# Kernel optimization log

Hardware: AMD Instinct MI355X
Metric: run time of the kernel (lower is better)

The kernel has to match this reference:

```python
import jax, jax.numpy as jnp
import numpy as np

B, C, H, W = 4, 256, 128, 256
CQK = C // 4   # 64
COUT = 256


def setup_inputs() -> dict:
    key = jax.random.key(0)
    ks = jax.random.split(key, 8)
    s = 0.05
    return {
        "flow": jax.random.normal(ks[0], (B, C, H, W), jnp.float32),
        "de_out": jax.random.normal(ks[1], (B, C, H, W), jnp.float32),
        "Wq": jax.random.normal(ks[2], (CQK, C), jnp.float32) * s,
        "bq": jax.random.normal(ks[3], (CQK,), jnp.float32) * s,
        "Wk": jax.random.normal(ks[4], (CQK, C), jnp.float32) * s,
        "bk": jax.random.normal(ks[5], (CQK,), jnp.float32) * s,
        "Wv": jax.random.normal(ks[6], (COUT, C), jnp.float32) * s,
        "bv": jax.random.normal(ks[7], (COUT,), jnp.float32) * s,
    }


def reference(flow, de_out, Wq, bq, Wk, bk, Wv, bv):
    # 1x1 convs == channel-mixing einsums
    q = jnp.einsum('bchw,dc->bdhw', de_out, Wq) + bq[None, :, None, None]  # [B,CQK,H,W]
    k = jnp.einsum('bchw,dc->bdhw', flow, Wk) + bk[None, :, None, None]   # [B,CQK,H,W]
    v = jnp.einsum('bchw,oc->bohw', flow, Wv) + bv[None, :, None, None]   # [B,COUT,H,W]
    # width-axial attention: energy[b,h,w,w'] = sum_d q[b,d,h,w]*k[b,d,h,w']
    energy = jnp.einsum('bdhw,bdhv->bhwv', q, k)          # [B,H,W,W]
    att = jax.nn.softmax(energy, axis=-1)                 # softmax over key width w'
    # out[b,o,h,w] = sum_{w'} v[b,o,h,w'] * att[b,h,w,w']
    out = jnp.einsum('bohv,bhwv->bohw', v, att)           # [B,COUT,H,W]
    return out
```

## Files before the change

kernel.cpp:

```cpp
#include <hip/hip_runtime.h>

#define Bn   4
#define Cc   256
#define Hh   128
#define Ww   256
#define HWp  32768
#define CQK  64
#define COUT 256

typedef _Float16 half8 __attribute__((ext_vector_type(8)));
typedef _Float16 half4 __attribute__((ext_vector_type(4)));
typedef float   floatx4 __attribute__((ext_vector_type(4)));

#define MFMA16(a, b, c) __builtin_amdgcn_mfma_f32_16x16x32_f16((a), (b), (c), 0, 0, 0)

__global__ __launch_bounds__(256) void k_qkv(
    const float* __restrict__ flow, const float* __restrict__ de_out,
    const float* __restrict__ Wq, const float* __restrict__ bq,
    const float* __restrict__ Wk, const float* __restrict__ bk,
    const float* __restrict__ Wv, const float* __restrict__ bv,
    _Float16* __restrict__ Qws, _Float16* __restrict__ Kws,
    _Float16* __restrict__ Vws)
{
    __shared__ __align__(16) _Float16 x_lds[64 * 264];
    __shared__ __align__(16) _Float16 w_lds[32 * 264];

    const int t   = threadIdx.x;
    const int b   = blockIdx.y;
    const int job = blockIdx.z;
    const int pb  = blockIdx.x * 64;

    const float* X = (job == 0 ? de_out : flow) + (size_t)b * Cc * HWp;

    {
        const int px4 = t & 15;
        const int cg  = t >> 4;
        for (int rep = 0; rep < 4; ++rep) {
            const int c0 = 4 * cg + 64 * rep;
            float4 r0 = *(const float4*)&X[(size_t)(c0 + 0) * HWp + pb + 4 * px4];
            float4 r1 = *(const float4*)&X[(size_t)(c0 + 1) * HWp + pb + 4 * px4];
            float4 r2 = *(const float4*)&X[(size_t)(c0 + 2) * HWp + pb + 4 * px4];
            float4 r3 = *(const float4*)&X[(size_t)(c0 + 3) * HWp + pb + 4 * px4];
            half4 h;
            h = (half4){(_Float16)r0.x, (_Float16)r1.x, (_Float16)r2.x, (_Float16)r3.x};
            *(half4*)&x_lds[(4 * px4 + 0) * 264 + c0] = h;
            h = (half4){(_Float16)r0.y, (_Float16)r1.y, (_Float16)r2.y, (_Float16)r3.y};
            *(half4*)&x_lds[(4 * px4 + 1) * 264 + c0] = h;
            h = (half4){(_Float16)r0.z, (_Float16)r1.z, (_Float16)r2.z, (_Float16)r3.z};
            *(half4*)&x_lds[(4 * px4 + 2) * 264 + c0] = h;
            h = (half4){(_Float16)r0.w, (_Float16)r1.w, (_Float16)r2.w, (_Float16)r3.w};
            *(half4*)&x_lds[(4 * px4 + 3) * 264 + c0] = h;
        }
    }

    const int nmt  = (job == 0) ? 2 : 10;
    const int wv   = t >> 6;
    const int lane = t & 63;
    const int quad = lane >> 4;
    const int l16  = lane & 15;

    for (int mt = 0; mt < nmt; ++mt) {
        const float* Wsel;
        const float* bsel;
        int mbase, dstmode;
        _Float16* dst;
        if (job == 0)      { Wsel = Wq; bsel = bq; mbase = mt * 32;        dst = Qws; dstmode = 0; }
        else if (mt < 2)   { Wsel = Wk; bsel = bk; mbase = mt * 32;        dst = Kws; dstmode = 0; }
        else               { Wsel = Wv; bsel = bv; mbase = (mt - 2) * 32;  dst = Vws; dstmode = 1; }

        __syncthreads();
        for (int i = 0; i < 8; ++i) {
            const int f4  = t + 256 * i;
            const int row = f4 >> 6;
            const int off = (f4 & 63) * 4;
            float4 w4 = *(const float4*)&Wsel[(size_t)(mbase + row) * 256 + off];
            half4 h = (half4){(_Float16)w4.x, (_Float16)w4.y, (_Float16)w4.z, (_Float16)w4.w};
            *(half4*)&w_lds[row * 264 + off] = h;
        }
        __syncthreads();

        const int mrow = 16 * (wv & 1) + l16;
        half8 a[8];
        for (int ks = 0; ks < 8; ++ks)
            a[ks] = *(const half8*)&w_lds[mrow * 264 + ks * 32 + quad * 8];

        const int n0 = (wv >> 1) * 32;
        floatx4 acc0 = {0.f, 0.f, 0.f, 0.f};
        floatx4 acc1 = {0.f, 0.f, 0.f, 0.f};
        for (int ks = 0; ks < 8; ++ks) {
            half8 b0 = *(const half8*)&x_lds[(n0 + l16) * 264 + ks * 32 + quad * 8];
            half8 b1 = *(const half8*)&x_lds[(n0 + 16 + l16) * 264 + ks * 32 + quad * 8];
            acc0 = MFMA16(a[ks], b0, acc0);
            acc1 = MFMA16(a[ks], b1, acc1);
        }

        const int mloc = 16 * (wv & 1) + quad * 4;
        float4 bi = *(const float4*)&bsel[mbase + mloc];
        const float bia[4] = {bi.x, bi.y, bi.z, bi.w};
        if (dstmode == 0) {
            for (int nt = 0; nt < 2; ++nt) {
                floatx4 acc = nt ? acc1 : acc0;
                const int pix = pb + n0 + nt * 16 + l16;
                half4 h = (half4){(_Float16)(acc[0] + bia[0]), (_Float16)(acc[1] + bia[1]),
                                  (_Float16)(acc[2] + bia[2]), (_Float16)(acc[3] + bia[3])};
                *(half4*)&dst[((size_t)b * HWp + pix) * 64 + mt * 32 + mloc] = h;
            }
        } else {
            for (int nt = 0; nt < 2; ++nt) {
                floatx4 acc = nt ? acc1 : acc0;
                const int pix = pb + n0 + nt * 16 + l16;
                for (int r = 0; r < 4; ++r) {
                    const int o = mbase + mloc + r;
                    dst[((size_t)b * 256 + o) * HWp + pix] = (_Float16)(acc[r] + bia[r]);
                }
            }
        }
    }
}

__global__ __launch_bounds__(256) void k_attn(
    const _Float16* __restrict__ Qws, const _Float16* __restrict__ Kws,
    const _Float16* __restrict__ Vws, float* __restrict__ out)
{
    __shared__ __align__(16) _Float16 q_lds[32 * 72];
    __shared__ __align__(16) _Float16 k_lds[256 * 72];
    __shared__ __align__(16) _Float16 att_lds[32 * 264];
    __shared__ float inv_l[32];

    const int t    = threadIdx.x;
    const int h    = blockIdx.x;
    const int b    = blockIdx.y;
    const int wv   = t >> 6;
    const int lane = t & 63;
    const int quad = lane >> 4;
    const int l16  = lane & 15;
    const size_t pixbase = (size_t)b * HWp + h * 256;

    for (int chunk = 0; chunk < 8; ++chunk) {
        __syncthreads();
        {
            const int row = t >> 3, off = (t & 7) * 8;
            *(half8*)&q_lds[row * 72 + off] =
                *(const half8*)&Qws[(pixbase + chunk * 32 + row) * 64 + off];
        }
        for (int i = 0; i < 8; ++i) {
            const int g = t + 256 * i;
            const int row = g >> 3, off = (g & 7) * 8;
            *(half8*)&k_lds[row * 72 + off] =
                *(const half8*)&Kws[(pixbase + row) * 64 + off];
        }
        __syncthreads();

        {
            const int mrow = 16 * (wv & 1) + l16;
            half8 a0 = *(const half8*)&q_lds[mrow * 72 + quad * 8];
            half8 a1 = *(const half8*)&q_lds[mrow * 72 + 32 + quad * 8];
            const int mb2 = 16 * (wv & 1) + quad * 4;
            for (int j = 0; j < 8; ++j) {
                const int nt = (wv >> 1) * 8 + j;
                half8 b0 = *(const half8*)&k_lds[(nt * 16 + l16) * 72 + quad * 8];
                half8 b1 = *(const half8*)&k_lds[(nt * 16 + l16) * 72 + 32 + quad * 8];
                floatx4 acc = {0.f, 0.f, 0.f, 0.f};
                acc = MFMA16(a0, b0, acc);
                acc = MFMA16(a1, b1, acc);
                for (int r = 0; r < 4; ++r)
                    att_lds[(mb2 + r) * 264 + nt * 16 + l16] = (_Float16)acc[r];
            }
        }
        __syncthreads();

        {
            const int r = t >> 3, seg = t & 7;
            _Float16* rowp = &att_lds[r * 264 + seg * 32];
            float vals[32];
            float mx = -1e30f;
            for (int i = 0; i < 32; ++i) { vals[i] = (float)rowp[i]; mx = fmaxf(mx, vals[i]); }
            mx = fmaxf(mx, __shfl_xor(mx, 1));
            mx = fmaxf(mx, __shfl_xor(mx, 2));
            mx = fmaxf(mx, __shfl_xor(mx, 4));
            float s = 0.f;
            for (int i = 0; i < 32; ++i) { vals[i] = __expf(vals[i] - mx); s += vals[i]; }
            s += __shfl_xor(s, 1);
            s += __shfl_xor(s, 2);
            s += __shfl_xor(s, 4);
            for (int i = 0; i < 32; ++i) rowp[i] = (_Float16)vals[i];
            if (seg == 0) inv_l[r] = 1.f / s;
        }
        __syncthreads();

        _Float16* v_lds = k_lds;
        for (int os = 0; os < 4; ++os) {
            if (os) __syncthreads();
            for (int i = 0; i < 8; ++i) {
                const int g = t + 256 * i;
                const int row = g >> 5, off = (g & 31) * 8;
                *(half8*)&v_lds[row * 264 + off] =
                    *(const half8*)&Vws[((size_t)b * 256 + os * 64 + row) * HWp + h * 256 + off];
            }
            __syncthreads();

            floatx4 acc0 = {0.f, 0.f, 0.f, 0.f};
            floatx4 acc1 = {0.f, 0.f, 0.f, 0.f};
            for (int ks = 0; ks < 8; ++ks) {
                half8 a  = *(const half8*)&v_lds[(16 * wv + l16) * 264 + ks * 32 + quad * 8];
                half8 b0 = *(const half8*)&att_lds[l16 * 264 + ks * 32 + quad * 8];
                half8 b1 = *(const half8*)&att_lds[(16 + l16) * 264 + ks * 32 + quad * 8];
                acc0 = MFMA16(a, b0, acc0);
                acc1 = MFMA16(a, b1, acc1);
            }
            const float il0 = inv_l[l16];
            const float il1 = inv_l[16 + l16];
            const int og = os * 64 + 16 * wv + quad * 4;
            const int wg = chunk * 32 + l16;
            for (int r = 0; r < 4; ++r) {
                out[(((size_t)b * 256 + og + r) * Hh + h) * Ww + wg]      = acc0[r] * il0;
                out[(((size_t)b * 256 + og + r) * Hh + h) * Ww + 16 + wg] = acc1[r] * il1;
            }
        }
    }
}

extern "C" void kernel_launch(void* const* d_in, const int* in_sizes, int n_in,
                              void* d_out, int out_size, void* d_ws, size_t ws_size,
                              hipStream_t stream)
{
    const float* flow   = (const float*)d_in[0];
    const float* de_out = (const float*)d_in[1];
    const float* Wq = (const float*)d_in[2];
    const float* bq = (const float*)d_in[3];
    const float* Wk = (const float*)d_in[4];
    const float* bk = (const float*)d_in[5];
    const float* Wv = (const float*)d_in[6];
    const float* bv = (const float*)d_in[7];

    _Float16* Qws = (_Float16*)d_ws;
    _Float16* Kws = Qws + (size_t)Bn * HWp * 64;
    _Float16* Vws = Kws + (size_t)Bn * HWp * 64;
    float* out = (float*)d_out;

    dim3 g1(HWp / 64, Bn, 2);
    k_qkv<<<g1, 256, 0, stream>>>(flow, de_out, Wq, bq, Wk, bk, Wv, bv, Qws, Kws, Vws);

    dim3 g2(Hh, Bn);
    k_attn<<<g2, 256, 0, stream>>>(Qws, Kws, Vws, out);
}
```

Before: 452.8 us.

## Use 32x32 MFMA and 64-row query chunks in attention, drop weight LDS staging in QKV

```diff
diff --git a/kernel.cpp b/kernel.cpp
--- a/kernel.cpp
+++ b/kernel.cpp
@@ -10,11 +10,13 @@
 
 typedef _Float16 half8 __attribute__((ext_vector_type(8)));
 typedef _Float16 half4 __attribute__((ext_vector_type(4)));
-typedef float   floatx4 __attribute__((ext_vector_type(4)));
+typedef float   floatx4  __attribute__((ext_vector_type(4)));
+typedef float   floatx16 __attribute__((ext_vector_type(16)));
 
 #define MFMA16(a, b, c) __builtin_amdgcn_mfma_f32_16x16x32_f16((a), (b), (c), 0, 0, 0)
-
-__global__ __launch_bounds__(256) void k_qkv(
+#define MFMA32(a, b, c) __builtin_amdgcn_mfma_f32_32x32x16_f16((a), (b), (c), 0, 0, 0)
+
+__global__ __launch_bounds__(256, 4) void k_qkv(
     const float* __restrict__ flow, const float* __restrict__ de_out,
     const float* __restrict__ Wq, const float* __restrict__ bq,
     const float* __restrict__ Wk, const float* __restrict__ bk,
@@ -23,7 +25,6 @@
     _Float16* __restrict__ Vws)
 {
     __shared__ __align__(16) _Float16 x_lds[64 * 264];
-    __shared__ __align__(16) _Float16 w_lds[32 * 264];
 
     const int t   = threadIdx.x;
     const int b   = blockIdx.y;
@@ -34,83 +35,65 @@
 
     {
         const int px4 = t & 15;
-        const int cg  = t >> 4;
-        for (int rep = 0; rep < 4; ++rep) {
-            const int c0 = 4 * cg + 64 * rep;
-            float4 r0 = *(const float4*)&X[(size_t)(c0 + 0) * HWp + pb + 4 * px4];
-            float4 r1 = *(const float4*)&X[(size_t)(c0 + 1) * HWp + pb + 4 * px4];
-            float4 r2 = *(const float4*)&X[(size_t)(c0 + 2) * HWp + pb + 4 * px4];
-            float4 r3 = *(const float4*)&X[(size_t)(c0 + 3) * HWp + pb + 4 * px4];
-            half4 h;
-            h = (half4){(_Float16)r0.x, (_Float16)r1.x, (_Float16)r2.x, (_Float16)r3.x};
-            *(half4*)&x_lds[(4 * px4 + 0) * 264 + c0] = h;
-            h = (half4){(_Float16)r0.y, (_Float16)r1.y, (_Float16)r2.y, (_Float16)r3.y};
-            *(half4*)&x_lds[(4 * px4 + 1) * 264 + c0] = h;
-            h = (half4){(_Float16)r0.z, (_Float16)r1.z, (_Float16)r2.z, (_Float16)r3.z};
-            *(half4*)&x_lds[(4 * px4 + 2) * 264 + c0] = h;
-            h = (half4){(_Float16)r0.w, (_Float16)r1.w, (_Float16)r2.w, (_Float16)r3.w};
-            *(half4*)&x_lds[(4 * px4 + 3) * 264 + c0] = h;
+        const int c8  = t >> 4;
+        for (int rep = 0; rep < 2; ++rep) {
+            const int c0 = 8 * c8 + 128 * rep;
+            float4 r[8];
+            #pragma unroll
+            for (int j = 0; j < 8; ++j)
+                r[j] = *(const float4*)&X[(size_t)(c0 + j) * HWp + pb + 4 * px4];
+            #pragma unroll
+            for (int i = 0; i < 4; ++i) {
+                half8 h;
+                #pragma unroll
+                for (int j = 0; j < 8; ++j) h[j] = (_Float16)((&r[j].x)[i]);
+                *(half8*)&x_lds[(4 * px4 + i) * 264 + c0] = h;
+            }
         }
     }
-
-    const int nmt  = (job == 0) ? 2 : 10;
+    __syncthreads();
+
     const int wv   = t >> 6;
     const int lane = t & 63;
     const int quad = lane >> 4;
     const int l16  = lane & 15;
-
-    for (int mt = 0; mt < nmt; ++mt) {
-        const float* Wsel;
-        const float* bsel;
-        int mbase, dstmode;
-        _Float16* dst;
-        if (job == 0)      { Wsel = Wq; bsel = bq; mbase = mt * 32;        dst = Qws; dstmode = 0; }
-        else if (mt < 2)   { Wsel = Wk; bsel = bk; mbase = mt * 32;        dst = Kws; dstmode = 0; }
-        else               { Wsel = Wv; bsel = bv; mbase = (mt - 2) * 32;  dst = Vws; dstmode = 1; }
-
-        __syncthreads();
-        for (int i = 0; i < 8; ++i) {
-            const int f4  = t + 256 * i;
-            const int row = f4 >> 6;
-            const int off = (f4 & 63) * 4;
-            float4 w4 = *(const float4*)&Wsel[(size_t)(mbase + row) * 256 + off];
-            half4 h = (half4){(_Float16)w4.x, (_Float16)w4.y, (_Float16)w4.z, (_Float16)w4.w};
-            *(half4*)&w_lds[row * 264 + off] = h;
-        }
-        __syncthreads();
-
-        const int mrow = 16 * (wv & 1) + l16;
+    const int ntiles = (job == 0) ? 1 : 5;
+
+    for (int tt = 0; tt < ntiles; ++tt) {
+        const float* Wsel; const float* bsel; _Float16* dst; int m0, mode;
+        if (job == 0)    { Wsel = Wq; bsel = bq; dst = Qws; m0 = 16 * wv;              mode = 0; }
+        else if (tt==0)  { Wsel = Wk; bsel = bk; dst = Kws; m0 = 16 * wv;              mode = 0; }
+        else             { Wsel = Wv; bsel = bv; dst = Vws; m0 = 64 * (tt-1) + 16*wv;  mode = 1; }
+
         half8 a[8];
-        for (int ks = 0; ks < 8; ++ks)
-            a[ks] = *(const half8*)&w_lds[mrow * 264 + ks * 32 + quad * 8];
-
-        const int n0 = (wv >> 1) * 32;
-        floatx4 acc0 = {0.f, 0.f, 0.f, 0.f};
-        floatx4 acc1 = {0.f, 0.f, 0.f, 0.f};
+        const float* wrow = &Wsel[(size_t)(m0 + l16) * 256];
+        #pragma unroll
         for (int ks = 0; ks < 8; ++ks) {
-            half8 b0 = *(const half8*)&x_lds[(n0 + l16) * 264 + ks * 32 + quad * 8];
-            half8 b1 = *(const half8*)&x_lds[(n0 + 16 + l16) * 264 + ks * 32 + quad * 8];
-            acc0 = MFMA16(a[ks], b0, acc0);
-            acc1 = MFMA16(a[ks], b1, acc1);
-        }
-
-        const int mloc = 16 * (wv & 1) + quad * 4;
-        float4 bi = *(const float4*)&bsel[mbase + mloc];
+            float4 wa = *(const float4*)&wrow[ks * 32 + quad * 8];
+            float4 wb = *(const float4*)&wrow[ks * 32 + quad * 8 + 4];
+            a[ks] = (half8){(_Float16)wa.x, (_Float16)wa.y, (_Float16)wa.z, (_Float16)wa.w,
+                            (_Float16)wb.x, (_Float16)wb.y, (_Float16)wb.z, (_Float16)wb.w};
+        }
+        float4 bi = *(const float4*)&bsel[m0 + quad * 4];
         const float bia[4] = {bi.x, bi.y, bi.z, bi.w};
-        if (dstmode == 0) {
-            for (int nt = 0; nt < 2; ++nt) {
-                floatx4 acc = nt ? acc1 : acc0;
-                const int pix = pb + n0 + nt * 16 + l16;
+
+        #pragma unroll
+        for (int nt = 0; nt < 4; ++nt) {
+            floatx4 acc = {0.f, 0.f, 0.f, 0.f};
+            #pragma unroll
+            for (int ks = 0; ks < 8; ++ks) {
+                half8 bf = *(const half8*)&x_lds[(nt * 16 + l16) * 264 + ks * 32 + quad * 8];
+                acc = MFMA16(a[ks], bf, acc);
+            }
+            const int pix = pb + nt * 16 + l16;
+            if (mode == 0) {
                 half4 h = (half4){(_Float16)(acc[0] + bia[0]), (_Float16)(acc[1] + bia[1]),
                                   (_Float16)(acc[2] + bia[2]), (_Float16)(acc[3] + bia[3])};
-                *(half4*)&dst[((size_t)b * HWp + pix) * 64 + mt * 32 + mloc] = h;
-            }
-        } else {
-            for (int nt = 0; nt < 2; ++nt) {
-                floatx4 acc = nt ? acc1 : acc0;
-                const int pix = pb + n0 + nt * 16 + l16;
+                *(half4*)&dst[((size_t)b * HWp + pix) * 64 + m0 + quad * 4] = h;
+            } else {
+                #pragma unroll
                 for (int r = 0; r < 4; ++r) {
-                    const int o = mbase + mloc + r;
+                    const int o = m0 + quad * 4 + r;
                     dst[((size_t)b * 256 + o) * HWp + pix] = (_Float16)(acc[r] + bia[r]);
                 }
             }
@@ -118,103 +101,124 @@
     }
 }
 
-__global__ __launch_bounds__(256) void k_attn(
+__global__ __launch_bounds__(256, 2) void k_attn(
     const _Float16* __restrict__ Qws, const _Float16* __restrict__ Kws,
     const _Float16* __restrict__ Vws, float* __restrict__ out)
 {
-    __shared__ __align__(16) _Float16 q_lds[32 * 72];
-    __shared__ __align__(16) _Float16 k_lds[256 * 72];
-    __shared__ __align__(16) _Float16 att_lds[32 * 264];
-    __shared__ float inv_l[32];
+    __shared__ __align__(16) _Float16 kv_lds[256 * 72];
+    __shared__ __align__(16) _Float16 att_lds[64 * 264];
+    __shared__ float inv_l[64];
 
     const int t    = threadIdx.x;
     const int h    = blockIdx.x;
     const int b    = blockIdx.y;
     const int wv   = t >> 6;
     const int lane = t & 63;
-    const int quad = lane >> 4;
-    const int l16  = lane & 15;
+    const int hi   = lane >> 5;
+    const int l32  = lane & 31;
     const size_t pixbase = (size_t)b * HWp + h * 256;
 
-    for (int chunk = 0; chunk < 8; ++chunk) {
-        __syncthreads();
-        {
-            const int row = t >> 3, off = (t & 7) * 8;
-            *(half8*)&q_lds[row * 72 + off] =
-                *(const half8*)&Qws[(pixbase + chunk * 32 + row) * 64 + off];
-        }
+    for (int chunk = 0; chunk < 4; ++chunk) {
+        __syncthreads();
+        #pragma unroll
         for (int i = 0; i < 8; ++i) {
             const int g = t + 256 * i;
             const int row = g >> 3, off = (g & 7) * 8;
-            *(half8*)&k_lds[row * 72 + off] =
+            *(half8*)&kv_lds[row * 72 + off] =
                 *(const half8*)&Kws[(pixbase + row) * 64 + off];
         }
         __syncthreads();
 
         {
-            const int mrow = 16 * (wv & 1) + l16;
-            half8 a0 = *(const half8*)&q_lds[mrow * 72 + quad * 8];
-            half8 a1 = *(const half8*)&q_lds[mrow * 72 + 32 + quad * 8];
-            const int mb2 = 16 * (wv & 1) + quad * 4;
-            for (int j = 0; j < 8; ++j) {
-                const int nt = (wv >> 1) * 8 + j;
-                half8 b0 = *(const half8*)&k_lds[(nt * 16 + l16) * 72 + quad * 8];
-                half8 b1 = *(const half8*)&k_lds[(nt * 16 + l16) * 72 + 32 + quad * 8];
-                floatx4 acc = {0.f, 0.f, 0.f, 0.f};
-                acc = MFMA16(a0, b0, acc);
-                acc = MFMA16(a1, b1, acc);
-                for (int r = 0; r < 4; ++r)
-                    att_lds[(mb2 + r) * 264 + nt * 16 + l16] = (_Float16)acc[r];
-            }
-        }
-        __syncthreads();
-
-        {
-            const int r = t >> 3, seg = t & 7;
-            _Float16* rowp = &att_lds[r * 264 + seg * 32];
+            const int mt = wv & 1;
+            half8 aq[4];
+            #pragma unroll
+            for (int ks = 0; ks < 4; ++ks)
+                aq[ks] = *(const half8*)&Qws[(pixbase + chunk*64 + mt*32 + l32) * 64
+                                             + ks * 16 + hi * 8];
+            #pragma unroll
+            for (int j = 0; j < 4; ++j) {
+                const int n0 = (4 * (wv >> 1) + j) * 32;
+                floatx16 acc = {};
+                #pragma unroll
+                for (int ks = 0; ks < 4; ++ks) {
+                    half8 bk8 = *(const half8*)&kv_lds[(n0 + l32) * 72 + ks * 16 + hi * 8];
+                    acc = MFMA32(aq[ks], bk8, acc);
+                }
+                #pragma unroll
+                for (int r = 0; r < 16; ++r) {
+                    const int row = mt * 32 + (r & 3) + 8 * (r >> 2) + 4 * hi;
+                    att_lds[row * 264 + n0 + l32] = (_Float16)acc[r];
+                }
+            }
+        }
+        __syncthreads();
+
+        #pragma unroll
+        for (int p = 0; p < 2; ++p) {
+            const int row = 32 * p + (t >> 3), seg = t & 7;
+            _Float16* rowp = &att_lds[row * 264 + seg * 32];
             float vals[32];
             float mx = -1e30f;
-            for (int i = 0; i < 32; ++i) { vals[i] = (float)rowp[i]; mx = fmaxf(mx, vals[i]); }
+            #pragma unroll
+            for (int i8 = 0; i8 < 4; ++i8) {
+                half8 hv = *(const half8*)&rowp[i8 * 8];
+                #pragma unroll
+                for (int j = 0; j < 8; ++j) {
+                    vals[i8 * 8 + j] = (float)hv[j];
+                    mx = fmaxf(mx, vals[i8 * 8 + j]);
+                }
+            }
             mx = fmaxf(mx, __shfl_xor(mx, 1));
             mx = fmaxf(mx, __shfl_xor(mx, 2));
             mx = fmaxf(mx, __shfl_xor(mx, 4));
             float s = 0.f;
+            #pragma unroll
             for (int i = 0; i < 32; ++i) { vals[i] = __expf(vals[i] - mx); s += vals[i]; }
             s += __shfl_xor(s, 1);
             s += __shfl_xor(s, 2);
             s += __shfl_xor(s, 4);
-            for (int i = 0; i < 32; ++i) rowp[i] = (_Float16)vals[i];
-            if (seg == 0) inv_l[r] = 1.f / s;
-        }
-        __syncthreads();
-
-        _Float16* v_lds = k_lds;
+            #pragma unroll
+            for (int i8 = 0; i8 < 4; ++i8) {
+                half8 hv;
+                #pragma unroll
+                for (int j = 0; j < 8; ++j) hv[j] = (_Float16)vals[i8 * 8 + j];
+                *(half8*)&rowp[i8 * 8] = hv;
+            }
+            if (seg == 0) inv_l[row] = 1.f / s;
+        }
+        __syncthreads();
+
+        const int wt = wv & 1, ot = wv >> 1;
+        half8 batt[16];
+        #pragma unroll
+        for (int ks = 0; ks < 16; ++ks)
+            batt[ks] = *(const half8*)&att_lds[(wt * 32 + l32) * 264 + ks * 16 + hi * 8];
+        const float il = inv_l[wt * 32 + l32];
+
         for (int os = 0; os < 4; ++os) {
-            if (os) __syncthreads();
+            __syncthreads();
+            #pragma unroll
             for (int i = 0; i < 8; ++i) {
                 const int g = t + 256 * i;
                 const int row = g >> 5, off = (g & 31) * 8;
-                *(half8*)&v_lds[row * 264 + off] =
-                    *(const half8*)&Vws[((size_t)b * 256 + os * 64 + row) * HWp + h * 256 + off];
+                *(half8*)&kv_lds[row * 264 + off] =
+                    *(const half8*)&Vws[((size_t)b * 256 + os * 64 + row) * HWp
+                                        + h * 256 + off];
             }
             __syncthreads();
 
-            floatx4 acc0 = {0.f, 0.f, 0.f, 0.f};
-            floatx4 acc1 = {0.f, 0.f, 0.f, 0.f};
-            for (int ks = 0; ks < 8; ++ks) {
-                half8 a  = *(const half8*)&v_lds[(16 * wv + l16) * 264 + ks * 32 + quad * 8];
-                half8 b0 = *(const half8*)&att_lds[l16 * 264 + ks * 32 + quad * 8];
-                half8 b1 = *(const half8*)&att_lds[(16 + l16) * 264 + ks * 32 + quad * 8];
-                acc0 = MFMA16(a, b0, acc0);
-                acc1 = MFMA16(a, b1, acc1);
-            }
-            const float il0 = inv_l[l16];
-            const float il1 = inv_l[16 + l16];
-            const int og = os * 64 + 16 * wv + quad * 4;
-            const int wg = chunk * 32 + l16;
-            for (int r = 0; r < 4; ++r) {
-                out[(((size_t)b * 256 + og + r) * Hh + h) * Ww + wg]      = acc0[r] * il0;
-                out[(((size_t)b * 256 + og + r) * Hh + h) * Ww + 16 + wg] = acc1[r] * il1;
+            floatx16 acc = {};
+            #pragma unroll
+            for (int ks = 0; ks < 16; ++ks) {
+                half8 av = *(const half8*)&kv_lds[(ot * 32 + l32) * 264 + ks * 16 + hi * 8];
+                acc = MFMA32(av, batt[ks], acc);
+            }
+            const int wgl = chunk * 64 + wt * 32 + l32;
+            #pragma unroll
+            for (int r = 0; r < 16; ++r) {
+                const int o = os * 64 + ot * 32 + (r & 3) + 8 * (r >> 2) + 4 * hi;
+                out[((size_t)(b * 256 + o) * Hh + h) * Ww + wgl] = acc[r] * il;
             }
         }
     }
```

Measured after the change: 504.5 us. 1.11x slower.
